# Kernel optimization log

Hardware: AMD Instinct MI355X
Metric: run time of the kernel (lower is better)

Reference implementation:

```python
import jax, jax.numpy as jnp
import numpy as np

B, N = 8, 256            # molecules, atoms per molecule (equal sizes)
BN = B * N               # total nodes
E = 16384                # total edges
H, NH, HD = 256, 8, 32   # hidden, heads, head_dim
VD = 8                   # (lmax+1)^2 - 1 with lmax=2
CUTOFF = 5.0


def setup_inputs() -> dict:
    key = jax.random.key(0)
    ks = jax.random.split(key, 24)
    s = 1.0 / np.sqrt(H)
    d_raw = jax.random.normal(ks[5], (E, VD), jnp.float32)
    d_ij = d_raw / (jnp.linalg.norm(d_raw, axis=1, keepdims=True) + 1e-8)
    return {
        'x': jax.random.normal(ks[0], (BN, H), jnp.float32),
        'vec': jax.random.normal(ks[1], (BN, VD, H), jnp.float32),
        'edge_index': jax.random.randint(ks[2], (2, E), 0, BN, jnp.int32),
        'r_ij': jax.random.uniform(ks[3], (E,), jnp.float32) * CUTOFF,
        'f_ij': jax.random.normal(ks[4], (E, H), jnp.float32),
        'd_ij': d_ij,
        'batch': jnp.arange(BN, dtype=jnp.int32) // N,
        'ln_w': jnp.ones((H,), jnp.float32),
        'ln_b': jnp.zeros((H,), jnp.float32),
        'Wq': jax.random.normal(ks[6], (H, H), jnp.float32) * s,
        'Wk': jax.random.normal(ks[7], (H, H), jnp.float32) * s,
        'Wv': jax.random.normal(ks[8], (H, H), jnp.float32) * s,
        'Wao': jax.random.normal(ks[9], (H, H), jnp.float32) * s,
        'Wvec': jax.random.normal(ks[10], (H, 2 * H), jnp.float32) * s,
        'Wdv': jax.random.normal(ks[11], (H, H), jnp.float32) * s,
        'bdv': jnp.zeros((H,), jnp.float32),
        'Ws': jax.random.normal(ks[12], (H, 2 * H), jnp.float32) * s,
        'bs': jnp.zeros((2 * H,), jnp.float32),
        'Wo': jax.random.normal(ks[13], (H, 3 * H), jnp.float32) * s,
        'bo': jnp.zeros((3 * H,), jnp.float32),
        'Wf': jax.random.normal(ks[14], (H, H), jnp.float32) * s,
        'bf': jnp.zeros((H,), jnp.float32),
        'Wsrc': jax.random.normal(ks[15], (H, H), jnp.float32) * s,
        'Wtrg': jax.random.normal(ks[16], (H, H), jnp.float32) * s,
    }


def _vector_rejection(v, d):
    # v: [E, VD, H], d: [E, VD]
    proj = (v * d[:, :, None]).sum(axis=1, keepdims=True)
    return v - proj * d[:, :, None]


def _layer(x, vec, edge_index, r_ij, f_ij, d_ij,
           ln_w, ln_b, Wq, Wk, Wv, Wao, Wvec, Wdv, bdv,
           Ws, bs, Wo, bo, Wf, bf, Wsrc, Wtrg):
    silu = jax.nn.silu
    # ---- LayerNorm on scalar features; VecLayerNorm('none', non-trainable) = identity
    mu = x.mean(-1, keepdims=True)
    var = ((x - mu) ** 2).mean(-1, keepdims=True)
    xn = (x - mu) / jnp.sqrt(var + 1e-5) * ln_w + ln_b

    # ---- 3-body padded attention (equal graph sizes -> mask is all-True)
    x_x = xn.reshape(B, N, H)
    q = (x_x @ Wq).reshape(B, N, NH, HD)
    k = (x_x @ Wk).reshape(B, N, NH, HD)
    vv = (x_x @ Wv).reshape(B, N, NH, HD)
    attn = silu(jnp.einsum('bihd,bjhd->bhij', q, k) / jnp.sqrt(jnp.float32(HD)))
    # mean over neighbor dim j fused into the contraction ( / N )
    v = (jnp.einsum('bhij,bjhd->bihd', attn, vv) / N).reshape(B, N, H) @ Wao
    v = v.reshape(BN, NH, HD)

    dv = silu(f_ij @ Wdv + bdv).reshape(E, NH, HD)
    vp = vec @ Wvec                       # [BN, VD, 2H]
    vec1, vec3 = vp[..., :H], vp[..., H:]
    vec_sum = vec1.sum(axis=1)            # [BN, H]

    # ---- message passing (source_to_target: gather at src, scatter-add at dst)
    src, dst = edge_index[0], edge_index[1]
    cut = 0.5 * (jnp.cos(jnp.pi * r_ij / CUTOFF) + 1.0) * (r_ij < CUTOFF)
    v_j = (v[src] * cut[:, None, None] * dv).reshape(E, H)
    s12 = silu(v_j @ Ws + bs)
    s1, s2 = s12[:, :H], s12[:, H:]
    vec_j = vec[src] * s1[:, None, :] + s2[:, None, :] * d_ij[:, :, None]
    x_agg = jax.ops.segment_sum(v_j, dst, num_segments=BN)
    vec_agg = jax.ops.segment_sum(vec_j, dst, num_segments=BN)

    o = x_agg @ Wo + bo
    o1, o2, o3 = o[:, :H], o[:, H:2 * H], o[:, 2 * H:]
    dx = vec_sum * o2 + o3
    dvec = vec3 * o1[:, None, :] + vec_agg

    # ---- edge update (not last layer)
    w1 = _vector_rejection(vec[dst] @ Wtrg, d_ij)
    w2 = _vector_rejection(vec[src] @ Wsrc, -d_ij)
    w_dot = (w1 * w2).sum(axis=1)         # [E, H]
    df_ij = silu(f_ij @ Wf + bf) * w_dot
    return dx, dvec, df_ij


def reference(x, vec, edge_index, r_ij, f_ij, d_ij, batch,
              ln_w, ln_b, Wq, Wk, Wv, Wao, Wvec, Wdv, bdv,
              Ws, bs, Wo, bo, Wf, bf, Wsrc, Wtrg):
    return _layer(x, vec, edge_index, r_ij, f_ij, d_ij,
                  ln_w, ln_b, Wq, Wk, Wv, Wao, Wvec, Wdv, bdv,
                  Ws, bs, Wo, bo, Wf, bf, Wsrc, Wtrg)
```

## Files before the change

kernel.cpp:

```cpp
#include <hip/hip_runtime.h>
#include <hip/hip_bf16.h>
#include <math.h>

typedef __hip_bfloat16 bf16;
#define DEV __device__ __forceinline__
DEV float silu_f(float x) { return x / (1.0f + __expf(-x)); }
DEV float toF(bf16 x) { return __bfloat162float(x); }
DEV void storeF(float* p, float v) { *p = v; }
DEV void storeF(bf16* p, float v) { *p = __float2bfloat16(v); }

constexpr int Bc = 8, Nc = 256, BNc = 2048, Ec = 16384;
constexpr int Hc = 256, NHc = 8, HDc = 32, VDc = 8;

typedef __attribute__((ext_vector_type(8))) short short8;
typedef __attribute__((ext_vector_type(4))) float floatx4;
union sh8 { short8 v; bf16 x[8]; };

DEV void async_copy16(const void* g, void* l) {
  __builtin_amdgcn_global_load_lds(
      (const __attribute__((address_space(1))) void*)g,
      (__attribute__((address_space(3))) void*)l, 16, 0, 0);
}


DEV void csr_body(const int* __restrict__ ei, int* __restrict__ rowptr,
                  int* __restrict__ eids, int* sm) {
  int* deg = sm;
  int* cur = sm + 2048;
  int* rp  = sm + 4096;
  int* ps  = sm + 6144;
  int t = threadIdx.x;
  for (int i = t; i < 2048; i += 256) { deg[i] = 0; cur[i] = 0; }
  __syncthreads();
#pragma unroll
  for (int rr = 0; rr < 2; ++rr) {
    int4 dv[8];
#pragma unroll
    for (int i = 0; i < 8; ++i)
      dv[i] = *(const int4*)&ei[Ec + ((rr * 8 + i) * 256 + t) * 4];
#pragma unroll
    for (int i = 0; i < 8; ++i) {
      atomicAdd(&deg[dv[i].x], 1); atomicAdd(&deg[dv[i].y], 1);
      atomicAdd(&deg[dv[i].z], 1); atomicAdd(&deg[dv[i].w], 1);
    }
  }
  __syncthreads();
  int loc[8], s = 0;
#pragma unroll
  for (int i = 0; i < 8; ++i) { loc[i] = s; s += deg[t * 8 + i]; }
  ps[t] = s;
  __syncthreads();
  for (int off = 1; off < 256; off <<= 1) {
    int v = (t >= off) ? ps[t - off] : 0;
    __syncthreads();
    ps[t] += v;
    __syncthreads();
  }
  int base = (t == 0) ? 0 : ps[t - 1];
#pragma unroll
  for (int i = 0; i < 8; ++i) {
    rp[t * 8 + i] = base + loc[i];
    rowptr[t * 8 + i] = base + loc[i];
  }
  if (t == 255) rowptr[2048] = Ec;
  __syncthreads();
#pragma unroll
  for (int rr = 0; rr < 2; ++rr) {
    int4 dv[8];
#pragma unroll
    for (int i = 0; i < 8; ++i)
      dv[i] = *(const int4*)&ei[Ec + ((rr * 8 + i) * 256 + t) * 4];
#pragma unroll
    for (int i = 0; i < 8; ++i) {
      int e0 = ((rr * 8 + i) * 256 + t) * 4;
      int p0 = atomicAdd(&cur[dv[i].x], 1); eids[rp[dv[i].x] + p0] = e0;
      int p1 = atomicAdd(&cur[dv[i].y], 1); eids[rp[dv[i].y] + p1] = e0 + 1;
      int p2 = atomicAdd(&cur[dv[i].z], 1); eids[rp[dv[i].z] + p2] = e0 + 2;
      int p3 = atomicAdd(&cur[dv[i].w], 1); eids[rp[dv[i].w] + p3] = e0 + 3;
    }
  }
}

struct WDesc { const float* in; bf16* out; int K, N; };

DEV void wprep_body(WDesc wd, int by, int bx, float* sm) {
  if (by * 32 >= wd.N) return;
  float (*t)[33] = (float (*)[33])sm;
  int k0 = bx * 32, n0 = by * 32;
  int tx = threadIdx.x & 31, ty = threadIdx.x >> 5;
#pragma unroll
  for (int i = 0; i < 32; i += 8)
    t[ty + i][tx] = wd.in[(size_t)(k0 + ty + i) * wd.N + n0 + tx];
  __syncthreads();
#pragma unroll
  for (int i = 0; i < 32; i += 8)
    wd.out[(size_t)(n0 + ty + i) * wd.K + k0 + tx] = __float2bfloat16(t[tx][ty + i]);
}

DEV void cvt_body(const float* __restrict__ in, bf16* __restrict__ out, int blk) {
  int i = (blk * 256 + threadIdx.x) * 4;
  float4 v = *(const float4*)&in[i];
  union { bf16 x[4]; uint2 u; } o;
  o.x[0] = __float2bfloat16(v.x); o.x[1] = __float2bfloat16(v.y);
  o.x[2] = __float2bfloat16(v.z); o.x[3] = __float2bfloat16(v.w);
  *(uint2*)&out[i] = o.u;
}

DEV void ln_body(const float* __restrict__ x, const float* __restrict__ w,
                 const float* __restrict__ b, bf16* __restrict__ xn,
                 int row, float* sm) {
  int h = threadIdx.x;
  float v = x[(size_t)row * Hc + h];
  sm[h] = v; __syncthreads();
  for (int s = 128; s > 0; s >>= 1) { if (h < s) sm[h] += sm[h + s]; __syncthreads(); }
  float mu = sm[0] * (1.0f / 256.0f);
  __syncthreads();
  float d = v - mu;
  sm[h] = d * d; __syncthreads();
  for (int s = 128; s > 0; s >>= 1) { if (h < s) sm[h] += sm[h + s]; __syncthreads(); }
  float var = sm[0] * (1.0f / 256.0f);
  float r = rsqrtf(var + 1e-5f);
  xn[(size_t)row * Hc + h] = __float2bfloat16(d * r * w[h] + b[h]);
}

template <int ACT, typename TC>
DEV void mgemm_body(const bf16* __restrict__ A, const bf16* __restrict__ Bt,
                    const float* __restrict__ bias, TC* __restrict__ C,
                    int M, int K, int N, int m0, int n0,
                    bf16* Als, bf16* Bls) {
  int tid = threadIdx.x;
  int lane = tid & 63, w = tid >> 6;
  int wm = (w & 1) * 64, wn = (w >> 1) * 64;
  int fm = lane & 15, g = lane >> 4;
  floatx4 acc[4][4] = {};
  for (int k0 = 0; k0 < K; k0 += 32) {
#pragma unroll
    for (int t = 0; t < 2; ++t) {
      int c = t * 256 + w * 64 + lane;
      int r = c >> 2, q = c & 3;
      bf16* ldsA = &Als[(t * 256 + w * 64) * 8 + lane * 8];
      bf16* ldsB = &Bls[(t * 256 + w * 64) * 8 + lane * 8];
      async_copy16(A + (size_t)(m0 + r) * K + k0 + q * 8, ldsA);
      async_copy16(Bt + (size_t)(n0 + r) * K + k0 + q * 8, ldsB);
    }
    __syncthreads();
    short8 af[4], bg[4];
#pragma unroll
    for (int i = 0; i < 4; ++i) {
      af[i] = *(const short8*)&Als[(wm + i * 16 + fm) * 32 + g * 8];
      bg[i] = *(const short8*)&Bls[(wn + i * 16 + fm) * 32 + g * 8];
    }
#pragma unroll
    for (int mi = 0; mi < 4; ++mi)
#pragma unroll
      for (int ni = 0; ni < 4; ++ni)
        acc[mi][ni] = __builtin_amdgcn_mfma_f32_16x16x32_bf16(
            af[mi], bg[ni], acc[mi][ni], 0, 0, 0);
    __syncthreads();
  }
#pragma unroll
  for (int mi = 0; mi < 4; ++mi) {
    int row0 = m0 + wm + mi * 16 + g * 4;
#pragma unroll
    for (int ni = 0; ni < 4; ++ni) {
      int col = n0 + wn + ni * 16 + fm;
      float bv = bias ? bias[col] : 0.0f;
#pragma unroll
      for (int r = 0; r < 4; ++r) {
        float v = acc[mi][ni][r] + bv;
        if (ACT) v = silu_f(v);
        storeF(&C[(size_t)(row0 + r) * N + col], v);
      }
    }
  }
}

DEV void xagg_body(const bf16* __restrict__ vj, const int* __restrict__ rowptr,
                   const int* __restrict__ eids, bf16* __restrict__ xagg, int blk) {
  int node = blk * 8 + (threadIdx.x >> 5);
  int tx = threadIdx.x & 31;
  float acc[8] = {};
  int lo = rowptr[node], hi = rowptr[node + 1];
  for (int i = lo; i < hi; ++i) {
    sh8 vv; vv.v = *(const short8*)&vj[(size_t)eids[i] * 256 + tx * 8];
#pragma unroll
    for (int c = 0; c < 8; ++c) acc[c] += toF(vv.x[c]);
  }
  sh8 o;
#pragma unroll
  for (int c = 0; c < 8; ++c) o.x[c] = __float2bfloat16(acc[c]);
  *(short8*)&xagg[(size_t)node * 256 + tx * 8] = o.v;
}

DEV void df_body(const bf16* __restrict__ vpT, const float* __restrict__ d_ij,
                 const bf16* __restrict__ fW, const int* __restrict__ ei,
                 float* __restrict__ out, int blk) {
  int te = threadIdx.x >> 5, tx = threadIdx.x & 31;
  int e = blk * 8 + te;
  int src = ei[e], dst = ei[Ec + e];
  float S[8] = {}, p1[8] = {}, p2[8] = {};
#pragma unroll
  for (int vd = 0; vd < 8; ++vd) {
    sh8 t1, t2;
    t1.v = *(const short8*)&vpT[((size_t)(dst * 8 + vd)) * 1024 + 512 + tx * 8];
    t2.v = *(const short8*)&vpT[((size_t)(src * 8 + vd)) * 1024 + 768 + tx * 8];
    float dd = d_ij[e * 8 + vd];
#pragma unroll
    for (int c = 0; c < 8; ++c) {
      float a = toF(t1.x[c]), b = toF(t2.x[c]);
      S[c] += a * b; p1[c] += a * dd; p2[c] += b * dd;
    }
  }
  sh8 fw; fw.v = *(const short8*)&fW[(size_t)e * 256 + tx * 8];
  float o[8];
#pragma unroll
  for (int c = 0; c < 8; ++c) o[c] = toF(fw.x[c]) * (S[c] - p1[c] * p2[c]);
  float* dst_p = &out[(size_t)e * 256 + tx * 8];
  *(float4*)dst_p = make_float4(o[0], o[1], o[2], o[3]);
  *(float4*)(dst_p + 4) = make_float4(o[4], o[5], o[6], o[7]);
}

DEV void dxsum_body(const bf16* __restrict__ vpT, const float* __restrict__ ob,
                    float* __restrict__ out, int blk) {
  int row = blk * 8 + (threadIdx.x >> 5);
  int tx = threadIdx.x & 31;
  float s[8] = {};
#pragma unroll
  for (int vd = 0; vd < 8; ++vd) {
    sh8 vv; vv.v = *(const short8*)&vpT[((size_t)(row * 8 + vd)) * 1024 + tx * 8];
#pragma unroll
    for (int c = 0; c < 8; ++c) s[c] += toF(vv.x[c]);
  }
  float4 o2a = *(const float4*)&ob[(size_t)row * 768 + 256 + tx * 8];
  float4 o2b = *(const float4*)&ob[(size_t)row * 768 + 260 + tx * 8];
  float4 o3a = *(const float4*)&ob[(size_t)row * 768 + 512 + tx * 8];
  float4 o3b = *(const float4*)&ob[(size_t)row * 768 + 516 + tx * 8];
  float o2[8] = {o2a.x, o2a.y, o2a.z, o2a.w, o2b.x, o2b.y, o2b.z, o2b.w};
  float o3[8] = {o3a.x, o3a.y, o3a.z, o3a.w, o3b.x, o3b.y, o3b.z, o3b.w};
  float r[8];
#pragma unroll
  for (int c = 0; c < 8; ++c) r[c] = s[c] * o2[c] + o3[c];
  float* dp = &out[(size_t)row * 256 + tx * 8];
  *(float4*)dp = make_float4(r[0], r[1], r[2], r[3]);
  *(float4*)(dp + 4) = make_float4(r[4], r[5], r[6], r[7]);
}

DEV void dvec_body(const bf16* __restrict__ vec_bf, const bf16* __restrict__ s12,
                   const float* __restrict__ d_ij, const int* __restrict__ ei,
                   const int* __restrict__ rowptr, const int* __restrict__ eids,
                   const bf16* __restrict__ vpT, const float* __restrict__ ob,
                   float* __restrict__ out, int n) {
  int tv = threadIdx.x >> 5, tx = threadIdx.x & 31;
  float acc[8] = {};
  int lo = rowptr[n], hi = rowptr[n + 1];
  for (int i = lo; i < hi; ++i) {
    int e = eids[i];
    int src = ei[e];
    sh8 s1, s2, vv;
    s1.v = *(const short8*)&s12[(size_t)e * 512 + tx * 8];
    s2.v = *(const short8*)&s12[(size_t)e * 512 + 256 + tx * 8];
    vv.v = *(const short8*)&vec_bf[((size_t)(src * 8 + tv)) * 256 + tx * 8];
    float dd = d_ij[e * 8 + tv];
#pragma unroll
    for (int c = 0; c < 8; ++c)
      acc[c] += toF(vv.x[c]) * toF(s1.x[c]) + toF(s2.x[c]) * dd;
  }
  sh8 v3; v3.v = *(const short8*)&vpT[((size_t)(n * 8 + tv)) * 1024 + 256 + tx * 8];
  float4 o1a = *(const float4*)&ob[(size_t)n * 768 + tx * 8];
  float4 o1b = *(const float4*)&ob[(size_t)n * 768 + 4 + tx * 8];
  float o1[8] = {o1a.x, o1a.y, o1a.z, o1a.w, o1b.x, o1b.y, o1b.z, o1b.w};
  float r[8];
#pragma unroll
  for (int c = 0; c < 8; ++c) r[c] = toF(v3.x[c]) * o1[c] + acc[c];
  float* dp = &out[((size_t)(n * 8 + tv)) * 256 + tx * 8];
  *(float4*)dp = make_float4(r[0], r[1], r[2], r[3]);
  *(float4*)(dp + 4) = make_float4(r[4], r[5], r[6], r[7]);
}


struct PrepArgs {
  const int* ei; int* rowptr; int* eids;
  WDesc wd[11];
  const float* f_ij; bf16* f_bf;
  const float* vec; bf16* vec_bf;
  const float* x; const float* ln_w; const float* ln_b; bf16* xn;
};

__global__ __launch_bounds__(256) void prep_k(PrepArgs a) {
  __shared__ __align__(16) char smem[25600];
  int blk = blockIdx.x;
  if (blk == 0) { csr_body(a.ei, a.rowptr, a.eids, (int*)smem); return; }
  blk -= 1;
  if (blk < 2112) { wprep_body(a.wd[blk / 192], (blk % 192) / 8, blk % 8, (float*)smem); return; }
  blk -= 2112;
  if (blk < 8192) {
    if (blk < 4096) cvt_body(a.f_ij, a.f_bf, blk);
    else cvt_body(a.vec, a.vec_bf, blk - 4096);
    return;
  }
  blk -= 8192;
  ln_body(a.x, a.ln_w, a.ln_b, a.xn, blk, (float*)smem);
}

struct G2Args {
  const bf16 *xn, *Wqkv, *vecbf, *Wvt;
  bf16 *qkv, *vpT;
};
__global__ __launch_bounds__(256) void gemm2_k(G2Args a) {
  __shared__ __align__(16) char smem[16384];
  bf16* Als = (bf16*)smem; bf16* Bls = (bf16*)(smem + 8192);
  int id = blockIdx.x;
  if (id < 96)
    mgemm_body<0, bf16>(a.xn, a.Wqkv, nullptr, a.qkv, BNc, Hc, 768,
                        (id % 16) * 128, (id / 16) * 128, Als, Bls);
  else {
    id -= 96;
    mgemm_body<0, bf16>(a.vecbf, a.Wvt, nullptr, a.vpT, Ec, Hc, 1024,
                        (id % 128) * 128, (id / 128) * 128, Als, Bls);
  }
}

__global__ __launch_bounds__(256) void attn_mfma_k(
    const bf16* __restrict__ qkv, bf16* __restrict__ ob) {
  constexpr int QS = 768;
  int b = blockIdx.x >> 3, h = blockIdx.x & 7;
  int tid = threadIdx.x, lane = tid & 63, w = tid >> 6;
  int fm = lane & 15, g = lane >> 4;
  __shared__ bf16 Vt[32][264];
  __shared__ bf16 Ps[4][64][72];
  const bf16* qb = qkv + (size_t)b * 256 * QS + h * 32;
  const bf16* kb = qb + 256;
  const bf16* vb = qb + 512;
#pragma unroll
  for (int c = 0; c < 4; ++c) {
    int chunk = c * 256 + tid;
    int j = chunk >> 2, part = chunk & 3;
    sh8 t;
    t.v = *(const short8*)(vb + (size_t)j * QS + part * 8);
#pragma unroll
    for (int i = 0; i < 8; ++i) Vt[part * 8 + i][j] = t.x[i];
  }
  __syncthreads();
  short8 af[4];
#pragma unroll
  for (int mi = 0; mi < 4; ++mi)
    af[mi] = *(const short8*)(qb + (size_t)(w * 64 + mi * 16 + fm) * QS + g * 8);
  floatx4 oacc[4][2] = {};
  for (int jt = 0; jt < 4; ++jt) {
#pragma unroll
    for (int ni = 0; ni < 4; ++ni) {
      short8 bg = *(const short8*)(kb + (size_t)(jt * 64 + ni * 16 + fm) * QS + g * 8);
#pragma unroll
      for (int mi = 0; mi < 4; ++mi) {
        floatx4 z = {0.f, 0.f, 0.f, 0.f};
        floatx4 s = __builtin_amdgcn_mfma_f32_16x16x32_bf16(af[mi], bg, z, 0, 0, 0);
#pragma unroll
        for (int r = 0; r < 4; ++r) {
          float v = silu_f(s[r] * 0.17677669529663687f);
          Ps[w][mi * 16 + g * 4 + r][ni * 16 + fm] = __float2bfloat16(v);
        }
      }
    }
#pragma unroll
    for (int kt = 0; kt < 2; ++kt) {
      short8 bv0 = *(const short8*)&Vt[fm][jt * 64 + kt * 32 + g * 8];
      short8 bv1 = *(const short8*)&Vt[16 + fm][jt * 64 + kt * 32 + g * 8];
#pragma unroll
      for (int mi = 0; mi < 4; ++mi) {
        short8 ap = *(const short8*)&Ps[w][mi * 16 + fm][kt * 32 + g * 8];
        oacc[mi][0] = __builtin_amdgcn_mfma_f32_16x16x32_bf16(ap, bv0, oacc[mi][0], 0, 0, 0);
        oacc[mi][1] = __builtin_amdgcn_mfma_f32_16x16x32_bf16(ap, bv1, oacc[mi][1], 0, 0, 0);
      }
    }
  }
#pragma unroll
  for (int mi = 0; mi < 4; ++mi)
#pragma unroll
    for (int ni = 0; ni < 2; ++ni)
#pragma unroll
      for (int r = 0; r < 4; ++r) {
        int row = w * 64 + mi * 16 + g * 4 + r;
        int d = ni * 16 + fm;
        ob[((size_t)(b * 256 + row)) * 256 + h * 32 + d] =
            __float2bfloat16(oacc[mi][ni][r] * (1.0f / 256.0f));
      }
}

template <int ACT, typename TC>
__global__ __launch_bounds__(256) void mgemm_k(
    const bf16* __restrict__ A, const bf16* __restrict__ Bt,
    const float* __restrict__ bias, TC* __restrict__ C,
    int M, int K, int N) {
  __shared__ __align__(16) char smem[16384];
  mgemm_body<ACT, TC>(A, Bt, bias, C, M, K, N,
                      blockIdx.x * 128, blockIdx.y * 128,
                      (bf16*)smem, (bf16*)(smem + 8192));
}

__global__ __launch_bounds__(256) void gemm_dvfw_k(
    const bf16* __restrict__ A, const bf16* __restrict__ Bt,
    const float* __restrict__ bdv, const float* __restrict__ bf_,
    const int* __restrict__ ei, const float* __restrict__ r_ij,
    const float* __restrict__ vbuf,
    bf16* __restrict__ vj, bf16* __restrict__ fW) {
  constexpr int K = 256;
  __shared__ __align__(16) char smem[16384];
  bf16* Als = (bf16*)smem; bf16* Bls = (bf16*)(smem + 8192);
  int tid = threadIdx.x;
  int lane = tid & 63, w = tid >> 6;
  int m0 = blockIdx.x * 128, n0 = blockIdx.y * 128;
  int wm = (w & 1) * 64, wn = (w >> 1) * 64;
  int fm = lane & 15, g = lane >> 4;
  floatx4 acc[4][4] = {};
  for (int k0 = 0; k0 < K; k0 += 32) {
#pragma unroll
    for (int t = 0; t < 2; ++t) {
      int c = t * 256 + w * 64 + lane;
      int r = c >> 2, q = c & 3;
      bf16* ldsA = &Als[(t * 256 + w * 64) * 8 + lane * 8];
      bf16* ldsB = &Bls[(t * 256 + w * 64) * 8 + lane * 8];
      async_copy16(A + (size_t)(m0 + r) * K + k0 + q * 8, ldsA);
      async_copy16(Bt + (size_t)(n0 + r) * K + k0 + q * 8, ldsB);
    }
    __syncthreads();
    short8 af[4], bg[4];
#pragma unroll
    for (int i = 0; i < 4; ++i) {
      af[i] = *(const short8*)&Als[(wm + i * 16 + fm) * 32 + g * 8];
      bg[i] = *(const short8*)&Bls[(wn + i * 16 + fm) * 32 + g * 8];
    }
#pragma unroll
    for (int mi = 0; mi < 4; ++mi)
#pragma unroll
      for (int ni = 0; ni < 4; ++ni)
        acc[mi][ni] = __builtin_amdgcn_mfma_f32_16x16x32_bf16(
            af[mi], bg[ni], acc[mi][ni], 0, 0, 0);
    __syncthreads();
  }
  bool isVj = (n0 < 256);
#pragma unroll
  for (int mi = 0; mi < 4; ++mi) {
    int row0 = m0 + wm + mi * 16 + g * 4;
#pragma unroll
    for (int r = 0; r < 4; ++r) {
      int e = row0 + r;
      int src = 0; float cut = 0.f;
      if (isVj) {
        src = ei[e];
        float rr = r_ij[e];
        cut = (rr < 5.0f) ? 0.5f * (cosf(0.6283185307179586f * rr) + 1.0f) : 0.0f;
      }
#pragma unroll
      for (int ni = 0; ni < 4; ++ni) {
        int col = n0 + wn + ni * 16 + fm;
        if (isVj) {
          float v = silu_f(acc[mi][ni][r] + bdv[col]);
          vj[(size_t)e * 256 + col] =
              __float2bfloat16(vbuf[(size_t)src * 256 + col] * cut * v);
        } else {
          float v = silu_f(acc[mi][ni][r] + bf_[col - 256]);
          fW[(size_t)e * 256 + (col - 256)] = __float2bfloat16(v);
        }
      }
    }
  }
}

struct S6Args {
  const bf16 *vj, *Ws_t; const float* bs; bf16* s12;
  const int *rowptr, *eids; bf16* xagg;
};
__global__ __launch_bounds__(256) void stage6_k(S6Args a) {
  __shared__ __align__(16) char smem[16384];
  int id = blockIdx.x;
  if (id < 512)
    mgemm_body<1, bf16>(a.vj, a.Ws_t, a.bs, a.s12, Ec, Hc, 512,
                        (id % 128) * 128, (id / 128) * 128,
                        (bf16*)smem, (bf16*)(smem + 8192));
  else
    xagg_body(a.vj, a.rowptr, a.eids, a.xagg, id - 512);
}

struct S7Args {
  const bf16 *xagg, *Wo_t; const float* bo; float* obuf;
  const bf16* vpT; const float* d_ij; const bf16* fW;
  const int* ei; float* out_df;
};
__global__ __launch_bounds__(256) void stage7_k(S7Args a) {
  __shared__ __align__(16) char smem[16384];
  int id = blockIdx.x;
  if (id < 96)
    mgemm_body<0, float>(a.xagg, a.Wo_t, a.bo, a.obuf, BNc, Hc, 768,
                         (id % 16) * 128, (id / 16) * 128,
                         (bf16*)smem, (bf16*)(smem + 8192));
  else
    df_body(a.vpT, a.d_ij, a.fW, a.ei, a.out_df, id - 96);
}

struct S8Args {
  const bf16* vpT; const float* obuf; float* out_dx;
  const bf16 *vecbf, *s12; const float* d_ij;
  const int *ei, *rowptr, *eids; float* out_dvec;
};
__global__ __launch_bounds__(256) void stage8_k(S8Args a) {
  int id = blockIdx.x;
  if (id < 256)
    dxsum_body(a.vpT, a.obuf, a.out_dx, id);
  else
    dvec_body(a.vecbf, a.s12, a.d_ij, a.ei, a.rowptr, a.eids,
              a.vpT, a.obuf, a.out_dvec, id - 256);
}

extern "C" void kernel_launch(void* const* d_in, const int* in_sizes, int n_in,
                              void* d_out, int out_size, void* d_ws, size_t ws_size,
                              hipStream_t stream) {
  const float* x    = (const float*)d_in[0];
  const float* vec  = (const float*)d_in[1];
  const int*   ei   = (const int*)d_in[2];
  const float* r_ij = (const float*)d_in[3];
  const float* f_ij = (const float*)d_in[4];
  const float* d_ij = (const float*)d_in[5];
  const float* ln_w = (const float*)d_in[7];
  const float* ln_b = (const float*)d_in[8];
  const float* Wq   = (const float*)d_in[9];
  const float* Wk   = (const float*)d_in[10];
  const float* Wv   = (const float*)d_in[11];
  const float* Wao  = (const float*)d_in[12];
  const float* Wvec = (const float*)d_in[13];
  const float* Wdv  = (const float*)d_in[14];
  const float* bdv  = (const float*)d_in[15];
  const float* Ws   = (const float*)d_in[16];
  const float* bs   = (const float*)d_in[17];
  const float* Wo   = (const float*)d_in[18];
  const float* bo   = (const float*)d_in[19];
  const float* Wf   = (const float*)d_in[20];
  const float* bf_  = (const float*)d_in[21];
  const float* Wsrc = (const float*)d_in[22];
  const float* Wtrg = (const float*)d_in[23];

  char* p = (char*)d_ws;
  auto alloc = [&](size_t bytes) {
    char* r = p; p += (bytes + 255) & ~(size_t)255; return r;
  };
  bf16*  xn_bf   = (bf16*)alloc((size_t)BNc * Hc * 2);
  bf16*  qkv_bf  = (bf16*)alloc((size_t)BNc * 3 * Hc * 2);
  bf16*  attn_bf = (bf16*)alloc((size_t)BNc * Hc * 2);
  float* vbuf    = (float*)alloc((size_t)BNc * Hc * 4);
  bf16*  xagg_bf = (bf16*)alloc((size_t)BNc * Hc * 2);
  float* obuf    = (float*)alloc((size_t)BNc * 3 * Hc * 4);
  bf16*  f_bf    = (bf16*)alloc((size_t)Ec * Hc * 2);
  bf16*  vec_bf  = (bf16*)alloc((size_t)BNc * VDc * Hc * 2);
  bf16*  vpT     = (bf16*)alloc((size_t)Ec * 1024 * 2);
  bf16*  vj_bf   = (bf16*)alloc((size_t)Ec * Hc * 2);
  bf16*  s12_bf  = (bf16*)alloc((size_t)Ec * 2 * Hc * 2);
  bf16*  fW_bf   = (bf16*)alloc((size_t)Ec * Hc * 2);
  bf16*  Wqkv_t  = (bf16*)alloc((size_t)3 * Hc * Hc * 2);
  bf16*  Wao_t   = (bf16*)alloc((size_t)Hc * Hc * 2);
  bf16*  Wdvf_t  = (bf16*)alloc((size_t)2 * Hc * Hc * 2);
  bf16*  Wvt_t   = (bf16*)alloc((size_t)4 * Hc * Hc * 2);
  bf16*  Ws_t    = (bf16*)alloc((size_t)2 * Hc * Hc * 2);
  bf16*  Wo_t    = (bf16*)alloc((size_t)3 * Hc * Hc * 2);
  int*   rowptr  = (int*)alloc(2049 * 4);
  int*   eids    = (int*)alloc(Ec * 4);

  float* out_dx   = (float*)d_out;
  float* out_dvec = (float*)d_out + 524288;
  float* out_df   = (float*)d_out + 4718592;

  PrepArgs pa;
  pa.ei = ei; pa.rowptr = rowptr; pa.eids = eids;
  pa.wd[0]  = {Wq,   Wqkv_t,           Hc, Hc};
  pa.wd[1]  = {Wk,   Wqkv_t + 65536,   Hc, Hc};
  pa.wd[2]  = {Wv,   Wqkv_t + 131072,  Hc, Hc};
  pa.wd[3]  = {Wao,  Wao_t,            Hc, Hc};
  pa.wd[4]  = {Wdv,  Wdvf_t,           Hc, Hc};
  pa.wd[5]  = {Wf,   Wdvf_t + 65536,   Hc, Hc};
  pa.wd[6]  = {Wvec, Wvt_t,            Hc, 2 * Hc};
  pa.wd[7]  = {Wtrg, Wvt_t + 131072,   Hc, Hc};
  pa.wd[8]  = {Wsrc, Wvt_t + 196608,   Hc, Hc};
  pa.wd[9]  = {Ws,   Ws_t,             Hc, 2 * Hc};
  pa.wd[10] = {Wo,   Wo_t,             Hc, 3 * Hc};
  pa.f_ij = f_ij; pa.f_bf = f_bf; pa.vec = vec; pa.vec_bf = vec_bf;
  pa.x = x; pa.ln_w = ln_w; pa.ln_b = ln_b; pa.xn = xn_bf;
  prep_k<<<12353, 256, 0, stream>>>(pa);

  G2Args g2{xn_bf, Wqkv_t, vec_bf, Wvt_t, qkv_bf, vpT};
  gemm2_k<<<1120, 256, 0, stream>>>(g2);

  attn_mfma_k<<<Bc * NHc, 256, 0, stream>>>(qkv_bf, attn_bf);

  mgemm_k<0, float><<<dim3(16, 2), 256, 0, stream>>>(attn_bf, Wao_t, nullptr, vbuf, BNc, Hc, Hc);

  gemm_dvfw_k<<<dim3(128, 4), 256, 0, stream>>>(f_bf, Wdvf_t, bdv, bf_, ei, r_ij,
                                                vbuf, vj_bf, fW_bf);

  S6Args s6{vj_bf, Ws_t, bs, s12_bf, rowptr, eids, xagg_bf};
  stage6_k<<<768, 256, 0, stream>>>(s6);

  S7Args s7{xagg_bf, Wo_t, bo, obuf, vpT, d_ij, fW_bf, ei, out_df};
  stage7_k<<<2144, 256, 0, stream>>>(s7);

  S8Args s8{vpT, obuf, out_dx, vec_bf, s12_bf, d_ij, ei, rowptr, eids, out_dvec};
  stage8_k<<<2304, 256, 0, stream>>>(s8);

  (void)in_sizes; (void)n_in; (void)out_size; (void)ws_size;
}
```

Baseline: 277.6 us.

## Regroup df by destination node and dvec by node-per-warp to reuse loads

Result: slower. 327.1 us (+17.8%).

```diff
diff --git a/kernel.cpp b/kernel.cpp
--- a/kernel.cpp
+++ b/kernel.cpp
@@ -192,32 +192,43 @@
   *(short8*)&xagg[(size_t)node * 256 + tx * 8] = o.v;
 }
 
-DEV void df_body(const bf16* __restrict__ vpT, const float* __restrict__ d_ij,
-                 const bf16* __restrict__ fW, const int* __restrict__ ei,
-                 float* __restrict__ out, int blk) {
-  int te = threadIdx.x >> 5, tx = threadIdx.x & 31;
-  int e = blk * 8 + te;
-  int src = ei[e], dst = ei[Ec + e];
-  float S[8] = {}, p1[8] = {}, p2[8] = {};
-#pragma unroll
-  for (int vd = 0; vd < 8; ++vd) {
-    sh8 t1, t2;
-    t1.v = *(const short8*)&vpT[((size_t)(dst * 8 + vd)) * 1024 + 512 + tx * 8];
-    t2.v = *(const short8*)&vpT[((size_t)(src * 8 + vd)) * 1024 + 768 + tx * 8];
-    float dd = d_ij[e * 8 + vd];
-#pragma unroll
-    for (int c = 0; c < 8; ++c) {
-      float a = toF(t1.x[c]), b = toF(t2.x[c]);
-      S[c] += a * b; p1[c] += a * dd; p2[c] += b * dd;
-    }
-  }
-  sh8 fw; fw.v = *(const short8*)&fW[(size_t)e * 256 + tx * 8];
-  float o[8];
-#pragma unroll
-  for (int c = 0; c < 8; ++c) o[c] = toF(fw.x[c]) * (S[c] - p1[c] * p2[c]);
-  float* dst_p = &out[(size_t)e * 256 + tx * 8];
-  *(float4*)dst_p = make_float4(o[0], o[1], o[2], o[3]);
-  *(float4*)(dst_p + 4) = make_float4(o[4], o[5], o[6], o[7]);
+DEV void df_node_body(const bf16* __restrict__ vpT, const float* __restrict__ d_ij,
+                      const bf16* __restrict__ fW, const int* __restrict__ ei,
+                      const int* __restrict__ rowptr, const int* __restrict__ eids,
+                      float* __restrict__ out, int node, bf16* lds ) {
+  int tid = threadIdx.x, te = tid >> 5, tx = tid & 31;
+  *(short8*)&lds[te * 256 + tx * 8] =
+      *(const short8*)&vpT[((size_t)(node * 8 + te)) * 1024 + 512 + tx * 8];
+  __syncthreads();
+  int lo = rowptr[node], hi = rowptr[node + 1];
+  for (int base = lo; base < hi; base += 8) {
+    int idx = base + te;
+    if (idx < hi) {
+      int e = eids[idx];
+      int src = ei[e];
+      float4 da = *(const float4*)&d_ij[e * 8];
+      float4 db = *(const float4*)&d_ij[e * 8 + 4];
+      float dd[8] = {da.x, da.y, da.z, da.w, db.x, db.y, db.z, db.w};
+      float S[8] = {}, p1[8] = {}, p2[8] = {};
+#pragma unroll
+      for (int vd = 0; vd < 8; ++vd) {
+        sh8 t1; t1.v = *(const short8*)&lds[vd * 256 + tx * 8];
+        sh8 t2; t2.v = *(const short8*)&vpT[((size_t)(src * 8 + vd)) * 1024 + 768 + tx * 8];
+#pragma unroll
+        for (int c = 0; c < 8; ++c) {
+          float a = toF(t1.x[c]), b = toF(t2.x[c]);
+          S[c] += a * b; p1[c] += a * dd[vd]; p2[c] += b * dd[vd];
+        }
+      }
+      sh8 fw; fw.v = *(const short8*)&fW[(size_t)e * 256 + tx * 8];
+      float o[8];
+#pragma unroll
+      for (int c = 0; c < 8; ++c) o[c] = toF(fw.x[c]) * (S[c] - p1[c] * p2[c]);
+      float* dp = &out[(size_t)e * 256 + tx * 8];
+      *(float4*)dp = make_float4(o[0], o[1], o[2], o[3]);
+      *(float4*)(dp + 4) = make_float4(o[4], o[5], o[6], o[7]);
+    }
+  }
 }
 
 DEV void dxsum_body(const bf16* __restrict__ vpT, const float* __restrict__ ob,
@@ -249,32 +260,41 @@
                    const float* __restrict__ d_ij, const int* __restrict__ ei,
                    const int* __restrict__ rowptr, const int* __restrict__ eids,
                    const bf16* __restrict__ vpT, const float* __restrict__ ob,
-                   float* __restrict__ out, int n) {
-  int tv = threadIdx.x >> 5, tx = threadIdx.x & 31;
-  float acc[8] = {};
+                   float* __restrict__ out, int blk) {
+  int tn = threadIdx.x >> 5, tx = threadIdx.x & 31;
+  int n = blk * 8 + tn;
+  float acc[8][8] = {};
   int lo = rowptr[n], hi = rowptr[n + 1];
   for (int i = lo; i < hi; ++i) {
     int e = eids[i];
     int src = ei[e];
-    sh8 s1, s2, vv;
+    sh8 s1, s2;
     s1.v = *(const short8*)&s12[(size_t)e * 512 + tx * 8];
     s2.v = *(const short8*)&s12[(size_t)e * 512 + 256 + tx * 8];
-    vv.v = *(const short8*)&vec_bf[((size_t)(src * 8 + tv)) * 256 + tx * 8];
-    float dd = d_ij[e * 8 + tv];
-#pragma unroll
-    for (int c = 0; c < 8; ++c)
-      acc[c] += toF(vv.x[c]) * toF(s1.x[c]) + toF(s2.x[c]) * dd;
-  }
-  sh8 v3; v3.v = *(const short8*)&vpT[((size_t)(n * 8 + tv)) * 1024 + 256 + tx * 8];
+    float4 da = *(const float4*)&d_ij[e * 8];
+    float4 db = *(const float4*)&d_ij[e * 8 + 4];
+    float dd[8] = {da.x, da.y, da.z, da.w, db.x, db.y, db.z, db.w};
+#pragma unroll
+    for (int vd = 0; vd < 8; ++vd) {
+      sh8 vv; vv.v = *(const short8*)&vec_bf[((size_t)(src * 8 + vd)) * 256 + tx * 8];
+#pragma unroll
+      for (int c = 0; c < 8; ++c)
+        acc[vd][c] += toF(vv.x[c]) * toF(s1.x[c]) + toF(s2.x[c]) * dd[vd];
+    }
+  }
   float4 o1a = *(const float4*)&ob[(size_t)n * 768 + tx * 8];
   float4 o1b = *(const float4*)&ob[(size_t)n * 768 + 4 + tx * 8];
   float o1[8] = {o1a.x, o1a.y, o1a.z, o1a.w, o1b.x, o1b.y, o1b.z, o1b.w};
-  float r[8];
-#pragma unroll
-  for (int c = 0; c < 8; ++c) r[c] = toF(v3.x[c]) * o1[c] + acc[c];
-  float* dp = &out[((size_t)(n * 8 + tv)) * 256 + tx * 8];
-  *(float4*)dp = make_float4(r[0], r[1], r[2], r[3]);
-  *(float4*)(dp + 4) = make_float4(r[4], r[5], r[6], r[7]);
+#pragma unroll
+  for (int vd = 0; vd < 8; ++vd) {
+    sh8 v3; v3.v = *(const short8*)&vpT[((size_t)(n * 8 + vd)) * 1024 + 256 + tx * 8];
+    float r[8];
+#pragma unroll
+    for (int c = 0; c < 8; ++c) r[c] = toF(v3.x[c]) * o1[c] + acc[vd][c];
+    float* dp = &out[((size_t)(n * 8 + vd)) * 256 + tx * 8];
+    *(float4*)dp = make_float4(r[0], r[1], r[2], r[3]);
+    *(float4*)(dp + 4) = make_float4(r[4], r[5], r[6], r[7]);
+  }
 }
 
 
@@ -484,7 +504,7 @@
 struct S7Args {
   const bf16 *xagg, *Wo_t; const float* bo; float* obuf;
   const bf16* vpT; const float* d_ij; const bf16* fW;
-  const int* ei; float* out_df;
+  const int *ei, *rowptr, *eids; float* out_df;
 };
 __global__ __launch_bounds__(256) void stage7_k(S7Args a) {
   __shared__ __align__(16) char smem[16384];
@@ -494,7 +514,8 @@
                          (id % 16) * 128, (id / 16) * 128,
                          (bf16*)smem, (bf16*)(smem + 8192));
   else
-    df_body(a.vpT, a.d_ij, a.fW, a.ei, a.out_df, id - 96);
+    df_node_body(a.vpT, a.d_ij, a.fW, a.ei, a.rowptr, a.eids,
+                 a.out_df, id - 96, (bf16*)smem);
 }
 
 struct S8Args {
@@ -597,11 +618,11 @@
   S6Args s6{vj_bf, Ws_t, bs, s12_bf, rowptr, eids, xagg_bf};
   stage6_k<<<768, 256, 0, stream>>>(s6);
 
-  S7Args s7{xagg_bf, Wo_t, bo, obuf, vpT, d_ij, fW_bf, ei, out_df};
+  S7Args s7{xagg_bf, Wo_t, bo, obuf, vpT, d_ij, fW_bf, ei, rowptr, eids, out_df};
   stage7_k<<<2144, 256, 0, stream>>>(s7);
 
   S8Args s8{vpT, obuf, out_dx, vec_bf, s12_bf, d_ij, ei, rowptr, eids, out_dvec};
-  stage8_k<<<2304, 256, 0, stream>>>(s8);
+  stage8_k<<<512, 256, 0, stream>>>(s8);
 
   (void)in_sizes; (void)n_in; (void)out_size; (void)ws_size;
 }
```
